# Kernel optimization log

Measured on AMD Instinct MI355X. Metric: run time of the kernel, lower is better.

The kernel has to match this reference:

```python
import jax, jax.numpy as jnp
import numpy as np

B, ENC_IN, ENC_HID, N, GH = 64, 64, 256, 2048, 128
LN_EPS = 1e-5


def _chain_adjacency(n):
    # tridiagonal chain adjacency, D^{-1/2} A D^{-1/2} normalized
    off = jnp.ones((n - 1,), dtype=jnp.float32)
    A = jnp.diag(off, 1) + jnp.diag(off, -1)
    deg = A.sum(axis=1)
    d_inv_sqrt = jnp.power(deg + 1e-8, -0.5)
    return A * d_inv_sqrt[None, :] * d_inv_sqrt[:, None]


def setup_inputs() -> dict:
    key = jax.random.key(0)
    ks = jax.random.split(key, 16)
    s = 0.02
    return {
        "x": jax.random.normal(ks[0], (B, ENC_IN), dtype=jnp.float32),
        "A_hat": _chain_adjacency(N),
        "W1": jax.random.normal(ks[1], (ENC_IN, ENC_HID), dtype=jnp.float32) * s,
        "b1": jnp.zeros((ENC_HID,), dtype=jnp.float32),
        "W2": jax.random.normal(ks[2], (ENC_HID, N * GH), dtype=jnp.float32) * s,
        "b2": jnp.zeros((N * GH,), dtype=jnp.float32),
        "Wg1": jax.random.normal(ks[3], (GH, GH), dtype=jnp.float32) * s,
        "Wg2": jax.random.normal(ks[4], (GH, GH), dtype=jnp.float32) * s,
        "ln_g1": jnp.ones((GH,), dtype=jnp.float32),
        "ln_b1": jnp.zeros((GH,), dtype=jnp.float32),
        "ln_g2": jnp.ones((GH,), dtype=jnp.float32),
        "ln_b2": jnp.zeros((GH,), dtype=jnp.float32),
        "Wout": jax.random.normal(ks[5], (GH, 1), dtype=jnp.float32) * s,
        "bout": jnp.zeros((1,), dtype=jnp.float32),
    }


def _layernorm(h, g, b):
    mu = h.mean(axis=-1, keepdims=True)
    var = ((h - mu) ** 2).mean(axis=-1, keepdims=True)
    return (h - mu) * jax.lax.rsqrt(var + LN_EPS) * g + b


def reference(x, A_hat, W1, b1, W2, b2, Wg1, Wg2, ln_g1, ln_b1, ln_g2, ln_b2, Wout, bout):
    # encoder MLP -> (B, N, GH) node features
    enc = jax.nn.relu(x @ W1 + b1) @ W2 + b2
    out = enc.reshape(B, N, GH)
    # GCN layers: out = out + A_hat @ (LN(out) W)   (dropout is identity at eval)
    for Wg, g, bb in ((Wg1, ln_g1, ln_b1), (Wg2, ln_g2, ln_b2)):
        h = _layernorm(out, g, bb)
        Wx = h @ Wg                              # (B, N, GH)
        out = out + jnp.einsum('ij,bjd->bid', A_hat, Wx)
    return (out @ Wout + bout).squeeze(-1)       # (B, N)
```

## Files before the change

### kernel.cpp

```cpp
#include <hip/hip_runtime.h>


#define B_    64
#define EIN   64
#define EHID  256
#define NN    2048
#define GH    128
#define NG    (NN*GH)
#define LN_EPS 1e-5f
#define C3    28
#define C4    128

typedef _Float16 f16;
typedef _Float16 f16x8 __attribute__((ext_vector_type(8)));
typedef _Float16 f16x4 __attribute__((ext_vector_type(4)));
typedef float    f32x4 __attribute__((ext_vector_type(4)));
typedef unsigned int u32;

__device__ __forceinline__ float wred(float v) {
#pragma unroll
    for (int off = 32; off > 0; off >>= 1) v += __shfl_xor(v, off, 64);
    return v;
}

__global__ __launch_bounds__(256) void k_prep(
    const float* __restrict__ x,  const float* __restrict__ W1, const float* __restrict__ b1,
    const float* __restrict__ Wg1,const float* __restrict__ Wg2,const float* __restrict__ Wout,
    f16* __restrict__ h1h, f16* __restrict__ wg1T, float* __restrict__ v2)
{
    int bid = blockIdx.x, tid = threadIdx.x;
    if (bid < 64) {
        int b = bid, j = tid;
        float acc = b1[j];
#pragma unroll 8
        for (int k = 0; k < EIN; ++k) acc = fmaf(x[b*EIN + k], W1[k*EHID + j], acc);
        h1h[b*EHID + j] = (f16)fmaxf(acc, 0.f);
    } else if (bid == 64) {
        if (tid < GH) {
            float s = 0.f;
            for (int j = 0; j < GH; ++j) s = fmaf(Wg2[tid*GH + j], Wout[j], s);
            v2[tid] = s;
        }
    } else {
        for (int i = tid; i < GH*GH; i += 256) {
            int n = i >> 7, k = i & 127;
            wg1T[i] = (f16)Wg1[k*GH + n];
        }
    }
}

__global__ __launch_bounds__(256) void k_enc(
    const float* __restrict__ W2, const float* __restrict__ b2,
    const f16* __restrict__ h1h, f16* __restrict__ out0)
{
    __shared__ f16 h1s[64][264];
    int tid = threadIdx.x;
    const u32* h1u = (const u32*)h1h;
    for (int i = tid; i < 8192; i += 256)
        ((u32*)h1s)[(i >> 7)*132 + (i & 127)] = h1u[i];
    __syncthreads();

    int L = tid & 63, wv = tid >> 6, hi = L >> 4, lo = L & 15;
    int c_lane = blockIdx.x*64 + wv*16 + lo;
    const float* Wp = W2 + c_lane;

    f32x4 z = {0.f, 0.f, 0.f, 0.f};
    f32x4 acc[4];
#pragma unroll
    for (int bg = 0; bg < 4; ++bg) acc[bg] = z;

#pragma unroll
    for (int kk = 0; kk < 8; ++kk) {
        f16x8 bf;
        const float* wr = Wp + (size_t)(kk*32 + hi*8) * NG;
#pragma unroll
        for (int j = 0; j < 8; ++j) bf[j] = (f16)wr[(size_t)j * NG];
#pragma unroll
        for (int bg = 0; bg < 4; ++bg) {
            f16x8 af = *(const f16x8*)&h1s[bg*16 + lo][kk*32 + hi*8];
            acc[bg] = __builtin_amdgcn_mfma_f32_16x16x32_f16(af, bf, acc[bg], 0, 0, 0);
        }
    }
    float bv = b2[c_lane];
#pragma unroll
    for (int bg = 0; bg < 4; ++bg)
#pragma unroll
        for (int r = 0; r < 4; ++r) {
            int brow = bg*16 + hi*4 + r;
            out0[(size_t)brow * NG + c_lane] = (f16)(acc[bg][r] + bv);
        }
}

__global__ __launch_bounds__(256) void k_gcn1(
    const float* __restrict__ A_hat, const float* __restrict__ ln_g1, const float* __restrict__ ln_b1,
    const f16* __restrict__ wg1T, const f16* __restrict__ out0, f16* __restrict__ out1)
{
    __shared__ f16 out0_s[32][132];
    __shared__ f16 h0s[32][136];
    __shared__ f16 wg1s[GH*GH];
    __shared__ f16 wx0_s[32][132];
    __shared__ float g1s[GH], b1s[GH];
    __shared__ float clo_s[C3], chi_s[C3];

    int tid = threadIdx.x;
    int n0 = blockIdx.x * C3;
    int b  = blockIdx.y;

    {
        const u32* wu = (const u32*)wg1T;
        u32* wd = (u32*)wg1s;
        for (int i = tid; i < 8192; i += 256) {
            int n = i >> 6, kp = i & 63;
            int cs = (kp >> 2) ^ (n & 15);
            wd[n*64 + cs*4 + (kp & 3)] = wu[i];
        }
    }
    for (int i = tid; i < 32*32; i += 256) {
        int r = i >> 5, gv = i & 31;
        int n = n0 - 2 + r;
        f16x4 v = {0, 0, 0, 0};
        if (n >= 0 && n < NN) v = *(const f16x4*)(out0 + ((size_t)b*NN + n)*GH + gv*4);
        *(f16x4*)&out0_s[r][gv*4] = v;
    }
    if (tid < GH) { g1s[tid] = ln_g1[tid]; b1s[tid] = ln_b1[tid]; }
    else if (tid < GH + C3) {
        int t = tid - GH, n = n0 + t;
        float cl = 0.f, ch = 0.f;
        if (n < NN) {
            if (n >= 1)    cl = A_hat[(size_t)n*NN + (n-1)];
            if (n <= NN-2) ch = A_hat[(size_t)n*NN + (n+1)];
        }
        clo_s[t] = cl; chi_s[t] = ch;
    }
    __syncthreads();

    int L = tid & 63, wv = tid >> 6, hi = L >> 4, lo = L & 15;
    for (int r = wv; r < 32; r += 4) {
        float x0 = (float)out0_s[r][2*L], x1 = (float)out0_s[r][2*L+1];
        float s  = wred(x0 + x1);
        float q  = wred(x0*x0 + x1*x1);
        float mu = s * (1.f/128.f);
        float inv = rsqrtf(q*(1.f/128.f) - mu*mu + LN_EPS);
        h0s[r][2*L]   = (f16)((x0 - mu)*inv*g1s[2*L]   + b1s[2*L]);
        h0s[r][2*L+1] = (f16)((x1 - mu)*inv*g1s[2*L+1] + b1s[2*L+1]);
    }
    __syncthreads();

    f32x4 z = {0.f, 0.f, 0.f, 0.f};
    f32x4 acc[2][2];
#pragma unroll
    for (int mg = 0; mg < 2; ++mg)
#pragma unroll
        for (int nt = 0; nt < 2; ++nt) acc[mg][nt] = z;

#pragma unroll
    for (int kk = 0; kk < 4; ++kk) {
        f16x8 af[2], bfr[2];
#pragma unroll
        for (int mg = 0; mg < 2; ++mg)
            af[mg] = *(const f16x8*)&h0s[mg*16 + lo][kk*32 + hi*8];
#pragma unroll
        for (int nt = 0; nt < 2; ++nt) {
            int n  = wv*32 + nt*16 + lo;
            int cs = (kk*4 + hi) ^ lo;
            bfr[nt] = *(const f16x8*)&wg1s[n*GH + cs*8];
        }
#pragma unroll
        for (int mg = 0; mg < 2; ++mg)
#pragma unroll
            for (int nt = 0; nt < 2; ++nt)
                acc[mg][nt] = __builtin_amdgcn_mfma_f32_16x16x32_f16(af[mg], bfr[nt], acc[mg][nt], 0, 0, 0);
    }
#pragma unroll
    for (int mg = 0; mg < 2; ++mg)
#pragma unroll
        for (int nt = 0; nt < 2; ++nt)
#pragma unroll
            for (int r = 0; r < 4; ++r)
                wx0_s[mg*16 + hi*4 + r][wv*32 + nt*16 + lo] = (f16)acc[mg][nt][r];
    __syncthreads();

    for (int i = tid; i < C3*GH; i += 256) {
        int t = i >> 7, g = i & 127;
        int n = n0 + t;
        if (n < NN) {
            float val = (float)out0_s[t+2][g]
                      + clo_s[t]*(float)wx0_s[t+1][g]
                      + chi_s[t]*(float)wx0_s[t+3][g];
            out1[((size_t)b*NN + n)*GH + g] = (f16)val;
        }
    }
}

__global__ __launch_bounds__(256) void k_gcn2(
    const float* __restrict__ A_hat, const float* __restrict__ ln_g2, const float* __restrict__ ln_b2,
    const float* __restrict__ Wout, const float* __restrict__ bout, const float* __restrict__ v2,
    const f16* __restrict__ out1, float* __restrict__ y)
{
    __shared__ f16 out1_s[C4+2][132];
    __shared__ float g2s[GH], b2s[GH], v2s[GH], wos[GH];
    __shared__ float ss[C4+2], yr[C4+2];

    int tid = threadIdx.x;
    int n0 = blockIdx.x * C4;
    int b  = blockIdx.y;

    for (int i = tid; i < (C4+2)*32; i += 256) {
        int r = i >> 5, gv = i & 31;
        int n = n0 - 1 + r;
        f16x4 v = {0, 0, 0, 0};
        if (n >= 0 && n < NN) v = *(const f16x4*)(out1 + ((size_t)b*NN + n)*GH + gv*4);
        *(f16x4*)&out1_s[r][gv*4] = v;
    }
    if (tid < GH) { g2s[tid] = ln_g2[tid]; b2s[tid] = ln_b2[tid]; v2s[tid] = v2[tid]; wos[tid] = Wout[tid]; }
    __syncthreads();

    int L = tid & 63, wv = tid >> 6;
    for (int r = wv; r < C4+2; r += 4) {
        float x0 = (float)out1_s[r][2*L], x1 = (float)out1_s[r][2*L+1];
        float s  = wred(x0 + x1);
        float q  = wred(x0*x0 + x1*x1);
        float mu = s * (1.f/128.f);
        float inv = rsqrtf(q*(1.f/128.f) - mu*mu + LN_EPS);
        float h0 = (x0 - mu)*inv*g2s[2*L]   + b2s[2*L];
        float h1 = (x1 - mu)*inv*g2s[2*L+1] + b2s[2*L+1];
        float sp = wred(h0*v2s[2*L] + h1*v2s[2*L+1]);
        float yp = wred(x0*wos[2*L] + x1*wos[2*L+1]);
        if (L == 0) { ss[r] = sp; yr[r] = yp; }
    }
    __syncthreads();

    if (tid < C4) {
        int n = n0 + tid, r = tid + 1;
        float cl = (n >= 1)    ? A_hat[(size_t)n*NN + (n-1)] : 0.f;
        float ch = (n <= NN-2) ? A_hat[(size_t)n*NN + (n+1)] : 0.f;
        y[(size_t)b*NN + n] = yr[r] + bout[0] + cl*ss[r-1] + ch*ss[r+1];
    }
}

extern "C" void kernel_launch(void* const* d_in, const int* in_sizes, int n_in,
                              void* d_out, int out_size, void* d_ws, size_t ws_size,
                              hipStream_t stream)
{
    (void)in_sizes; (void)n_in; (void)out_size; (void)ws_size;
    const float* x    = (const float*)d_in[0];
    const float* A_hat= (const float*)d_in[1];
    const float* W1   = (const float*)d_in[2];
    const float* b1   = (const float*)d_in[3];
    const float* W2   = (const float*)d_in[4];
    const float* b2   = (const float*)d_in[5];
    const float* Wg1  = (const float*)d_in[6];
    const float* Wg2  = (const float*)d_in[7];
    const float* g1   = (const float*)d_in[8];
    const float* lb1  = (const float*)d_in[9];
    const float* g2   = (const float*)d_in[10];
    const float* lb2  = (const float*)d_in[11];
    const float* Wout = (const float*)d_in[12];
    const float* bout = (const float*)d_in[13];
    float* y = (float*)d_out;

    char* ws = (char*)d_ws;
    f16*   h1h  = (f16*)(ws + 0);
    f16*   wg1T = (f16*)(ws + 32768);
    float* v2   = (float*)(ws + 65536);
    f16*   out0 = (f16*)(ws + (1u << 20));
    f16*   out1 = (f16*)(ws + (1u << 20) + (size_t)B_*NG*2);

    k_prep<<<dim3(66),                    256, 0, stream>>>(x, W1, b1, Wg1, Wg2, Wout, h1h, wg1T, v2);
    k_enc <<<dim3(NG/64),                 256, 0, stream>>>(W2, b2, h1h, out0);
    k_gcn1<<<dim3((NN + C3 - 1)/C3, B_),  256, 0, stream>>>(A_hat, g1, lb1, wg1T, out0, out1);
    k_gcn2<<<dim3(NN/C4, B_),             256, 0, stream>>>(A_hat, g2, lb2, Wout, bout, v2, out1, y);
}
```

Before: 537.0 us.

## Stream W2 tiles into LDS via async global_load_lds and drop weight staging in gcn1

The encoder GEMM now copies W2 tiles into double-buffered shared memory with the direct global-to-LDS load builtin, prefetching the next K slice while the current one feeds MFMA. Each block now covers 128 columns instead of 64, and h1 is read straight from global memory instead of being staged. k_gcn1 no longer copies Wg1 into swizzled shared memory and reads its B fragments from global/L2, which cuts LDS use and setup work per block. The aim is better coalescing of the dominant 128MB W2 read and less per-block overhead, at the cost of more sync points and uncached-in-LDS weight reads.

New measurement: 500.1 us. 1.07x faster.

```diff
diff --git a/kernel.cpp b/kernel.cpp
--- a/kernel.cpp
+++ b/kernel.cpp
@@ -16,6 +16,9 @@
 typedef _Float16 f16x4 __attribute__((ext_vector_type(4)));
 typedef float    f32x4 __attribute__((ext_vector_type(4)));
 typedef unsigned int u32;
+
+#define AS1 __attribute__((address_space(1)))
+#define AS3 __attribute__((address_space(3)))
 
 __device__ __forceinline__ float wred(float v) {
 #pragma unroll
@@ -53,42 +56,68 @@
     const float* __restrict__ W2, const float* __restrict__ b2,
     const f16* __restrict__ h1h, f16* __restrict__ out0)
 {
-    __shared__ f16 h1s[64][264];
+    __shared__ float w2s[2][32][128];
+
     int tid = threadIdx.x;
-    const u32* h1u = (const u32*)h1h;
-    for (int i = tid; i < 8192; i += 256)
-        ((u32*)h1s)[(i >> 7)*132 + (i & 127)] = h1u[i];
-    __syncthreads();
-
     int L = tid & 63, wv = tid >> 6, hi = L >> 4, lo = L & 15;
-    int c_lane = blockIdx.x*64 + wv*16 + lo;
-    const float* Wp = W2 + c_lane;
-
-    f32x4 z = {0.f, 0.f, 0.f, 0.f};
-    f32x4 acc[4];
-#pragma unroll
-    for (int bg = 0; bg < 4; ++bg) acc[bg] = z;
+    int c0 = blockIdx.x * 128;
+    int lrow = L >> 5, lcol4 = (L & 31) * 4;
+
+    auto stage = [&](int kk, int nb) {
+#pragma unroll
+        for (int s = 0; s < 4; ++s) {
+            int r = wv*8 + s*2;
+            const float* gp = W2 + (size_t)(kk*32 + r + lrow) * NG + c0 + lcol4;
+            __builtin_amdgcn_global_load_lds((const AS1 void*)gp,
+                                             (AS3 void*)&w2s[nb][r][0], 16, 0, 0);
+        }
+    };
+
+    stage(0, 0);
+
+    f32x4 acc[4][2];
+#pragma unroll
+    for (int bg = 0; bg < 4; ++bg)
+#pragma unroll
+        for (int t = 0; t < 2; ++t) acc[bg][t] = f32x4{0.f, 0.f, 0.f, 0.f};
 
 #pragma unroll
     for (int kk = 0; kk < 8; ++kk) {
-        f16x8 bf;
-        const float* wr = Wp + (size_t)(kk*32 + hi*8) * NG;
-#pragma unroll
-        for (int j = 0; j < 8; ++j) bf[j] = (f16)wr[(size_t)j * NG];
-#pragma unroll
-        for (int bg = 0; bg < 4; ++bg) {
-            f16x8 af = *(const f16x8*)&h1s[bg*16 + lo][kk*32 + hi*8];
-            acc[bg] = __builtin_amdgcn_mfma_f32_16x16x32_f16(af, bf, acc[bg], 0, 0, 0);
-        }
-    }
-    float bv = b2[c_lane];
+        __syncthreads();
+        if (kk < 7) stage(kk + 1, (kk + 1) & 1);
+
+        const float (*wb)[128] = w2s[kk & 1];
+        f16x8 bf[2];
+#pragma unroll
+        for (int t = 0; t < 2; ++t)
+#pragma unroll
+            for (int j = 0; j < 8; ++j)
+                bf[t][j] = (f16)wb[hi*8 + j][wv*32 + t*16 + lo];
+
+        f16x8 af[4];
+#pragma unroll
+        for (int bg = 0; bg < 4; ++bg)
+            af[bg] = *(const f16x8*)(h1h + ((bg*16 + lo) << 8) + kk*32 + hi*8);
+
+#pragma unroll
+        for (int bg = 0; bg < 4; ++bg)
+#pragma unroll
+            for (int t = 0; t < 2; ++t)
+                acc[bg][t] = __builtin_amdgcn_mfma_f32_16x16x32_f16(af[bg], bf[t], acc[bg][t], 0, 0, 0);
+    }
+
+    float bv[2];
+#pragma unroll
+    for (int t = 0; t < 2; ++t) bv[t] = b2[c0 + wv*32 + t*16 + lo];
 #pragma unroll
     for (int bg = 0; bg < 4; ++bg)
 #pragma unroll
-        for (int r = 0; r < 4; ++r) {
-            int brow = bg*16 + hi*4 + r;
-            out0[(size_t)brow * NG + c_lane] = (f16)(acc[bg][r] + bv);
-        }
+        for (int t = 0; t < 2; ++t)
+#pragma unroll
+            for (int r = 0; r < 4; ++r) {
+                int brow = bg*16 + hi*4 + r;
+                out0[(size_t)brow * NG + c0 + wv*32 + t*16 + lo] = (f16)(acc[bg][t][r] + bv[t]);
+            }
 }
 
 __global__ __launch_bounds__(256) void k_gcn1(
@@ -97,7 +126,6 @@
 {
     __shared__ f16 out0_s[32][132];
     __shared__ f16 h0s[32][136];
-    __shared__ f16 wg1s[GH*GH];
     __shared__ f16 wx0_s[32][132];
     __shared__ float g1s[GH], b1s[GH];
     __shared__ float clo_s[C3], chi_s[C3];
@@ -106,15 +134,6 @@
     int n0 = blockIdx.x * C3;
     int b  = blockIdx.y;
 
-    {
-        const u32* wu = (const u32*)wg1T;
-        u32* wd = (u32*)wg1s;
-        for (int i = tid; i < 8192; i += 256) {
-            int n = i >> 6, kp = i & 63;
-            int cs = (kp >> 2) ^ (n & 15);
-            wd[n*64 + cs*4 + (kp & 3)] = wu[i];
-        }
-    }
     for (int i = tid; i < 32*32; i += 256) {
         int r = i >> 5, gv = i & 31;
         int n = n0 - 2 + r;
@@ -161,9 +180,8 @@
             af[mg] = *(const f16x8*)&h0s[mg*16 + lo][kk*32 + hi*8];
 #pragma unroll
         for (int nt = 0; nt < 2; ++nt) {
-            int n  = wv*32 + nt*16 + lo;
-            int cs = (kk*4 + hi) ^ lo;
-            bfr[nt] = *(const f16x8*)&wg1s[n*GH + cs*8];
+            int n = wv*32 + nt*16 + lo;
+            bfr[nt] = *(const f16x8*)(wg1T + n*GH + kk*32 + hi*8);
         }
 #pragma unroll
         for (int mg = 0; mg < 2; ++mg)
@@ -267,7 +285,7 @@
     f16*   out1 = (f16*)(ws + (1u << 20) + (size_t)B_*NG*2);
 
     k_prep<<<dim3(66),                    256, 0, stream>>>(x, W1, b1, Wg1, Wg2, Wout, h1h, wg1T, v2);
-    k_enc <<<dim3(NG/64),                 256, 0, stream>>>(W2, b2, h1h, out0);
+    k_enc <<<dim3(NG/128),                256, 0, stream>>>(W2, b2, h1h, out0);
     k_gcn1<<<dim3((NN + C3 - 1)/C3, B_),  256, 0, stream>>>(A_hat, g1, lb1, wg1T, out0, out1);
     k_gcn2<<<dim3(NN/C4, B_),             256, 0, stream>>>(A_hat, g2, lb2, Wout, bout, v2, out1, y);
 }
```
